# Optimization experiments

Hardware: AMD Instinct MI355X
Metric: run time of the kernel (lower is better)

## Reference

```python
import jax, jax.numpy as jnp
import numpy as np

B, S, H, W, C = 1, 14, 56, 56, 192
WS = 7            # cubic window
SH = 3            # shift
HEADS = 6
HD = C // HEADS
N = WS ** 3       # 343 tokens per window
NW = (S // WS) * (H // WS) * (W // WS)  # 128 windows
SCALE = HD ** -0.5
HID = 4 * C
TBL = (2 * WS - 1) ** 3  # 2197


def _rel_index():
    # faithful to torch: meshgrid with indexing='xy' and the (3*ws-1)/(2*ws-1) strides
    c = np.stack(np.meshgrid(np.arange(WS), np.arange(WS), np.arange(WS), indexing='xy'))
    f = c.reshape(3, -1)                      # (3, N)
    r = (f[:, :, None] - f[:, None, :]).transpose(1, 2, 0)  # (N, N, 3)
    r = r + (WS - 1)
    r[..., 0] *= 3 * WS - 1
    r[..., 1] *= 2 * WS - 1
    return jnp.asarray(r.sum(-1), dtype=jnp.int32)  # (N, N)

REL_IDX = _rel_index()


def _ln(x, g, b):
    m = x.mean(-1, keepdims=True)
    v = ((x - m) ** 2).mean(-1, keepdims=True)
    return (x - m) * jax.lax.rsqrt(v + 1e-5) * g + b


def _partition(x):  # (B,S,H,W,C) -> (B*nW, N, C)
    x = x.reshape(B, S // WS, WS, H // WS, WS, W // WS, WS, C)
    x = x.transpose(0, 1, 3, 5, 2, 4, 6, 7)
    return x.reshape(-1, N, C)


def _reverse(w):  # (B*nW, N, C) -> (B,S,H,W,C)
    x = w.reshape(B, S // WS, H // WS, W // WS, WS, WS, WS, C)
    x = x.transpose(0, 1, 4, 2, 5, 3, 6, 7)
    return x.reshape(B, S, H, W, C)


def setup_inputs() -> dict:
    key = jax.random.key(0)
    ks = jax.random.split(key, 16)
    L = S * H * W
    p = lambda k, shp, s=0.02: (jax.random.normal(k, shp, dtype=jnp.float32) * s)
    return {
        'x': jax.random.normal(ks[0], (B, L, C), dtype=jnp.float32),
        'mask_matrix': jax.random.normal(ks[1], (NW, N, N), dtype=jnp.float32),
        'skip': jax.random.normal(ks[2], (B, L, C), dtype=jnp.float32),
        'x_up': jax.random.normal(ks[3], (B, L, C), dtype=jnp.float32),
        'norm1_g': jnp.ones((C,), jnp.float32),
        'norm1_b': jnp.zeros((C,), jnp.float32),
        'kv_w': p(ks[4], (C, 2 * C)),
        'kv_b': jnp.zeros((2 * C,), jnp.float32),
        'rel_bias_table': p(ks[5], (TBL, HEADS)),
        'proj_w': p(ks[6], (C, C)),
        'proj_b': jnp.zeros((C,), jnp.float32),
        'norm2_g': jnp.ones((C,), jnp.float32),
        'norm2_b': jnp.zeros((C,), jnp.float32),
        'fc1_w': p(ks[7], (C, HID)),
        'fc1_b': jnp.zeros((HID,), jnp.float32),
        'fc2_w': p(ks[8], (HID, C)),
        'fc2_b': jnp.zeros((C,), jnp.float32),
    }


def reference(x, mask_matrix, skip, x_up, norm1_g, norm1_b, kv_w, kv_b,
              rel_bias_table, proj_w, proj_b, norm2_g, norm2_b,
              fc1_w, fc1_b, fc2_w, fc2_b):
    shortcut = x
    sk = _ln(skip, norm1_g, norm1_b).reshape(B, S, H, W, C)
    xu = _ln(x_up, norm1_g, norm1_b).reshape(B, S, H, W, C)
    # cyclic shift (shift_size > 0, dims divisible by window -> no padding)
    sk = jnp.roll(sk, (-SH, -SH, -SH), axis=(1, 2, 3))
    xu = jnp.roll(xu, (-SH, -SH, -SH), axis=(1, 2, 3))
    sk_w = _partition(sk)   # (Bw, N, C)
    xu_w = _partition(xu)
    Bw = sk_w.shape[0]
    kv = (sk_w @ kv_w + kv_b).reshape(Bw, N, 2, HEADS, HD)
    k = kv[:, :, 0].transpose(0, 2, 1, 3)   # (Bw, h, N, d)
    v = kv[:, :, 1].transpose(0, 2, 1, 3)
    q = xu_w.reshape(Bw, N, HEADS, HD).transpose(0, 2, 1, 3) * SCALE
    attn = jnp.einsum('bhnd,bhmd->bhnm', q, k)
    bias = rel_bias_table[REL_IDX].transpose(2, 0, 1)  # (h, N, N)
    attn = attn + bias[None]
    attn = attn.reshape(B, NW, HEADS, N, N) + mask_matrix[None, :, None]
    attn = jax.nn.softmax(attn.reshape(Bw, HEADS, N, N), axis=-1)
    out = jnp.einsum('bhnm,bhmd->bhnd', attn, v)
    out = out.transpose(0, 2, 1, 3).reshape(Bw, N, C)
    out = out @ proj_w + proj_b
    xr = _reverse(out)
    xr = jnp.roll(xr, (SH, SH, SH), axis=(1, 2, 3)).reshape(B, S * H * W, C)
    x = shortcut + xr
    h = _ln(x, norm2_g, norm2_b)
    h = jax.nn.gelu(h @ fc1_w + fc1_b, approximate=False) @ fc2_w + fc2_b
    return x + h
```

## Files before the change

### kernel.cpp

```cpp
#include <hip/hip_runtime.h>
#include <cstddef>

typedef unsigned short u16;
typedef unsigned int   u32;
typedef __bf16 bf16_t;
typedef bf16_t bf16x8 __attribute__((ext_vector_type(8)));
typedef short  s16x4  __attribute__((ext_vector_type(4)));
typedef float  f32x4  __attribute__((ext_vector_type(4)));
typedef u16    u16x4  __attribute__((ext_vector_type(4)));

#define NPAD 352
#define VTS  352
#define LOG2E 1.4426950408889634f
#define RESCALE_THR 11.5f

__device__ __forceinline__ u16 f2b(float f) {
  return __builtin_bit_cast(u16, (__bf16)f);
}
__device__ __forceinline__ float b2f(u16 h) {
  return __uint_as_float(((u32)h) << 16);
}
__device__ __forceinline__ float fexp2(float x) {
#if __has_builtin(__builtin_amdgcn_exp2f)
  return __builtin_amdgcn_exp2f(x);
#else
  float r; asm("v_exp_f32 %0, %1" : "=v"(r) : "v"(x)); return r;
#endif
}
__device__ __forceinline__ f32x4 mfma16(bf16x8 a, bf16x8 b, f32x4 c) {
  return __builtin_amdgcn_mfma_f32_16x16x32_bf16(a, b, c, 0, 0, 0);
}
__device__ __forceinline__ f32x4 mfma16x16(s16x4 a, s16x4 b, f32x4 c) {
#if __has_builtin(__builtin_amdgcn_mfma_f32_16x16x16bf16_1k)
  return __builtin_amdgcn_mfma_f32_16x16x16bf16_1k(a, b, c, 0, 0, 0);
#else
  f32x4 d;
  asm volatile("v_mfma_f32_16x16x16_bf16 %0, %1, %2, %3"
               : "=&v"(d) : "v"(a), "v"(b), "v"(c));
  return d;
#endif
}
__device__ __forceinline__ void gl_lds16(const void* g, void* l) {
  __builtin_amdgcn_global_load_lds((const __attribute__((address_space(1))) void*)g,
                                   (__attribute__((address_space(3))) void*)l, 16, 0, 0);
}

__device__ __forceinline__ int win_to_global(int w, int n) {
  int ws = w >> 6, wh = (w >> 3) & 7, ww = w & 7;
  int ts = (n * 1338) >> 16;
  int rem = n - ts * 49;
  int th = (rem * 9363) >> 16;
  int tw = rem - th * 7;
  int gs = ws * 7 + ts + 3; if (gs >= 14) gs -= 14;
  int gh = wh * 7 + th + 3; if (gh >= 56) gh -= 56;
  int gw = ww * 7 + tw + 3; if (gw >= 56) gw -= 56;
  return (gs * 56 + gh) * 56 + gw;
}

#define MC_END 15488
#define LN_END (MC_END + 10976)
#define WC_END (LN_END + 1824)
#define PRE_GRID (WC_END + 726)

__global__ __launch_bounds__(256) void k_pre(
    const float* __restrict__ mask, u16* __restrict__ mb,
    const float* __restrict__ skip, const float* __restrict__ xup,
    const float* __restrict__ g1, const float* __restrict__ b1,
    u16* __restrict__ skw, u16* __restrict__ qb,
    const float* __restrict__ kv_w, const float* __restrict__ proj_w,
    const float* __restrict__ fc1_w, const float* __restrict__ fc2_w,
    u16* kvT, u16* projT, u16* fc1T, u16* fc2T,
    const float* __restrict__ tbl, u16* __restrict__ bf) {
  int bid = blockIdx.x, tid = threadIdx.x;
  if (bid < MC_END) {
    int t = bid * 256 + tid;
    int w = t / (352 * 88);
    int r = t - w * (352 * 88);
    int n = r / 88;
    int q = r - n * 88;
    u16x4 v = {0, 0, 0, 0};
    if (n < 343) {
      const float* src = mask + ((size_t)w * 343 + n) * 343 + q * 4;
      #pragma unroll
      for (int j = 0; j < 4; ++j) if (q * 4 + j < 343) v[j] = f2b(src[j] * LOG2E);
    }
    *(u16x4*)&mb[((size_t)w * 352 + n) * 352 + q * 4] = v;
  } else if (bid < LN_END) {
    int wid = tid >> 6, lane = tid & 63;
    int m = (bid - MC_END) * 4 + wid;
    u32 w = ((u32)m * 48914u) >> 24;
    int n = m - (int)w * 343;
    int g = win_to_global((int)w, n);
    float xs[3], xu[3];
    float s1 = 0.f, s2 = 0.f, t1 = 0.f, t2 = 0.f;
    #pragma unroll
    for (int i = 0; i < 3; ++i) {
      int c = lane + i * 64;
      xs[i] = skip[(size_t)g * 192 + c];
      xu[i] = xup[(size_t)g * 192 + c];
      s1 += xs[i]; s2 += xs[i] * xs[i];
      t1 += xu[i]; t2 += xu[i] * xu[i];
    }
    #pragma unroll
    for (int off = 1; off < 64; off <<= 1) {
      s1 += __shfl_xor(s1, off); s2 += __shfl_xor(s2, off);
      t1 += __shfl_xor(t1, off); t2 += __shfl_xor(t2, off);
    }
    const float inv = 1.f / 192.f;
    float ms = s1 * inv, vs = s2 * inv - ms * ms;
    float mu = t1 * inv, vu = t2 * inv - mu * mu;
    float rs = rsqrtf(vs + 1e-5f), ru = rsqrtf(vu + 1e-5f);
    #pragma unroll
    for (int i = 0; i < 3; ++i) {
      int c = lane + i * 64;
      float gg = g1[c], bb = b1[c];
      skw[(size_t)m * 192 + c] = f2b((xs[i] - ms) * rs * gg + bb);
      float qv = ((xu[i] - mu) * ru * gg + bb) * 0.25503513f;
      int h = c >> 5, d = c & 31;
      qb[(size_t)(((int)w * 6 + h) * NPAD + n) * 32 + d] = f2b(qv);
    }
  } else if (bid < WC_END) {
    int t = (bid - LN_END) * 256 + tid;
    if (t < 384 * 192) { int nn = t / 192, kk = t - nn * 192; kvT[t] = f2b(kv_w[kk * 384 + nn]); return; }
    t -= 384 * 192;
    if (t < 256 * 192) { int nn = t / 192, kk = t - nn * 192; projT[t] = (nn < 192) ? f2b(proj_w[kk * 192 + nn]) : (u16)0; return; }
    t -= 256 * 192;
    if (t < 768 * 192) { int nn = t / 192, kk = t - nn * 192; fc1T[t] = f2b(fc1_w[kk * 768 + nn]); return; }
    t -= 768 * 192;
    if (t < 256 * 768) { int nn = t / 768, kk = t - nn * 768; fc2T[t] = (nn < 192) ? f2b(fc2_w[kk * 192 + nn]) : (u16)0; return; }
  } else {
    int t = (bid - WC_END) * 256 + tid;
    int h = t / (352 * 88);
    int r = t - h * (352 * 88);
    int n = r / 88;
    int q = r - n * 88;
    u16x4 v = {0, 0, 0, 0};
    if (n < 343 && h < 6) {
      int tsn = (n * 1338) >> 16, remn = n - tsn * 49, thn = (remn * 9363) >> 16, twn = remn - thn * 7;
      #pragma unroll
      for (int j = 0; j < 4; ++j) {
        int m = q * 4 + j;
        if (m < 343) {
          int tsm = (m * 1338) >> 16, remm = m - tsm * 49, thm = (remm * 9363) >> 16, twm = remm - thm * 7;
          int idx = (thn - thm) * 20 + (tsn - tsm) * 13 + (twn - twm) + 204;
          v[j] = f2b(tbl[idx * 6 + h] * LOG2E);
        }
      }
    }
    if (h < 6) *(u16x4*)&bf[((size_t)h * 352 + n) * 352 + q * 4] = v;
  }
}

__global__ __launch_bounds__(256) void k_ln2(const float* __restrict__ xr,
    const float* __restrict__ g2, const float* __restrict__ b2, u16* __restrict__ o) {
  int wid = threadIdx.x >> 6, lane = threadIdx.x & 63;
  int m = blockIdx.x * 4 + wid;
  float v[3]; float s1 = 0.f, s2 = 0.f;
  #pragma unroll
  for (int i = 0; i < 3; ++i) {
    int c = lane + i * 64;
    v[i] = xr[(size_t)m * 192 + c];
    s1 += v[i]; s2 += v[i] * v[i];
  }
  #pragma unroll
  for (int off = 1; off < 64; off <<= 1) { s1 += __shfl_xor(s1, off); s2 += __shfl_xor(s2, off); }
  const float inv = 1.f / 192.f;
  float ms = s1 * inv, vs = s2 * inv - ms * ms;
  float rs = rsqrtf(vs + 1e-5f);
  #pragma unroll
  for (int i = 0; i < 3; ++i) {
    int c = lane + i * 64;
    o[(size_t)m * 192 + c] = f2b((v[i] - ms) * rs * g2[c] + b2[c]);
  }
}

template<int EPI>
__global__ __launch_bounds__(256) void k_gemm(
    const u16* __restrict__ A, const u16* __restrict__ Bm, int K, int nbn,
    const float* __restrict__ bias,
    u16* __restrict__ outa, u16* __restrict__ outb,
    const float* __restrict__ xin, float* __restrict__ xres,
    float* __restrict__ outf) {
  __shared__ __align__(16) u16 As[128 * 64];
  __shared__ __align__(16) u16 Bs[128 * 64];
  int bid = blockIdx.x;
  int xcd = bid & 7, j = bid >> 3;
  int bn = j % nbn, bmL = j / nbn;
  int bm = xcd * 43 + bmL;
  if (bm >= 343) return;
  int tid = threadIdx.x;
  int wid = tid >> 6, lane = tid & 63, lr = lane & 15, lg = lane >> 4;
  int wr = wid >> 1, wc = wid & 1;
  f32x4 acc[4][4] = {};
  const u16* Abase = A + (size_t)bm * 128 * K;
  const u16* Bbase = Bm + (size_t)bn * 128 * K;
  int nk = K >> 6;
  int rsw = lr & 7;
  for (int kt = 0; kt < nk; ++kt) {
    #pragma unroll
    for (int it = 0; it < 4; ++it) {
      int c = it * 256 + tid;
      int row = c >> 3, subp = c & 7;
      int gsub = subp ^ (row & 7);
      gl_lds16(Abase + (size_t)row * K + kt * 64 + gsub * 8, &As[c * 8]);
      gl_lds16(Bbase + (size_t)row * K + kt * 64 + gsub * 8, &Bs[c * 8]);
    }
    __syncthreads();
    #pragma unroll
    for (int kk = 0; kk < 2; ++kk) {
      bf16x8 af[4], bfr[4];
      #pragma unroll
      for (int mi = 0; mi < 4; ++mi)
        af[mi] = *(const bf16x8*)&As[(wr * 64 + mi * 16 + lr) * 64 + ((kk * 4 + lg) ^ rsw) * 8];
      #pragma unroll
      for (int ni = 0; ni < 4; ++ni)
        bfr[ni] = *(const bf16x8*)&Bs[(wc * 64 + ni * 16 + lr) * 64 + ((kk * 4 + lg) ^ rsw) * 8];
      #pragma unroll
      for (int mi = 0; mi < 4; ++mi)
        #pragma unroll
        for (int ni = 0; ni < 4; ++ni)
          acc[mi][ni] = mfma16(af[mi], bfr[ni], acc[mi][ni]);
    }
    __syncthreads();
  }
  #pragma unroll
  for (int mi = 0; mi < 4; ++mi) {
    #pragma unroll
    for (int r = 0; r < 4; ++r) {
      int grow = bm * 128 + wr * 64 + mi * 16 + lg * 4 + r;
      if (EPI == 0) {
        u32 w = ((u32)grow * 48914u) >> 24; int n = grow - (int)w * 343;
        #pragma unroll
        for (int ni = 0; ni < 4; ++ni) {
          int gcol = bn * 128 + wc * 64 + ni * 16 + lr;
          float v = acc[mi][ni][r] + bias[gcol];
          if (gcol < 192) {
            int hh = gcol >> 5, d = gcol & 31;
            int dswz = ((((d >> 3) ^ ((n >> 1) & 3)) << 3) | (d & 7));
            outa[(size_t)(((int)w * 6 + hh) * NPAD + n) * 32 + dswz] = f2b(v);
          } else {
            int c2 = gcol - 192; int hh = c2 >> 5, d = c2 & 31;
            int nswz = ((((n >> 3) ^ ((d >> 1) & 3)) << 3) | (n & 7));
            outb[(size_t)(((int)w * 6 + hh) * 32 + d) * VTS + nswz] = f2b(v);
          }
        }
      } else if (EPI == 1) {
        #pragma unroll
        for (int ni = 0; ni < 4; ++ni) {
          int gcol = bn * 128 + wc * 64 + ni * 16 + lr;
          if (gcol < 192) {
            float v = acc[mi][ni][r] + bias[gcol] + xin[(size_t)grow * 192 + gcol];
            xres[(size_t)grow * 192 + gcol] = v;
          }
        }
      } else if (EPI == 2) {
        #pragma unroll
        for (int ni = 0; ni < 4; ++ni) {
          int gcol = bn * 128 + wc * 64 + ni * 16 + lr;
          float v = acc[mi][ni][r] + bias[gcol];
          v = 0.5f * v * (1.f + erff(v * 0.7071067811865476f));
          outa[(size_t)grow * 768 + gcol] = f2b(v);
        }
      } else {
        #pragma unroll
        for (int ni = 0; ni < 4; ++ni) {
          int gcol = bn * 128 + wc * 64 + ni * 16 + lr;
          if (gcol < 192)
            outf[(size_t)grow * 192 + gcol] = acc[mi][ni][r] + bias[gcol] + xin[(size_t)grow * 192 + gcol];
        }
      }
    }
  }
}

template<int CT0, int LEN, bool TAIL, bool FIRST>
__device__ __forceinline__ void attn_chunk(const u16* __restrict__ Ks, const u16* __restrict__ Vs,
    bf16x8 qa, int lr, int lg, int swz,
    const u16* __restrict__ brow, const u16* __restrict__ mrow,
    f32x4& o0, f32x4& o1, float& mrun, float& sum) {
  u16x4 bb[LEN], mm[LEN];
  #pragma unroll
  for (int j = 0; j < LEN; ++j) {
    bb[j] = *(const u16x4*)&brow[(CT0 + j) * 16];
    mm[j] = *(const u16x4*)&mrow[(CT0 + j) * 16];
  }
  f32x4 s[LEN];
  const f32x4 z = {0.f, 0.f, 0.f, 0.f};
  __builtin_amdgcn_s_setprio(1);
  #pragma unroll
  for (int j = 0; j < LEN; ++j) {
    bf16x8 kf = *(const bf16x8*)&Ks[((CT0 + j) * 16 + lr) * 32 + (lg ^ swz) * 8];
    s[j] = mfma16(kf, qa, z);
  }
  __builtin_amdgcn_s_setprio(0);
  #pragma unroll
  for (int j = 0; j < LEN; ++j)
    #pragma unroll
    for (int r = 0; r < 4; ++r) s[j][r] += b2f(bb[j][r]) + b2f(mm[j][r]);
  if (TAIL) {
    int m0 = 336 + lg * 4;
    #pragma unroll
    for (int r = 0; r < 4; ++r) if (m0 + r >= 343) s[LEN - 1][r] = -1e30f;
  }
  float mloc = -1e30f;
  #pragma unroll
  for (int j = 0; j < LEN; ++j)
    mloc = fmaxf(mloc, fmaxf(fmaxf(s[j][0], s[j][1]), fmaxf(s[j][2], s[j][3])));
  if (FIRST) {
    mloc = fmaxf(mloc, __shfl_xor(mloc, 16));
    mloc = fmaxf(mloc, __shfl_xor(mloc, 32));
    mrun = mloc;
  } else if (!__all(mloc <= mrun + RESCALE_THR)) {
    mloc = fmaxf(mloc, __shfl_xor(mloc, 16));
    mloc = fmaxf(mloc, __shfl_xor(mloc, 32));
    float mnew = fmaxf(mrun, mloc);
    float sc = fexp2(mrun - mnew);
    #pragma unroll
    for (int r = 0; r < 4; ++r) {
      float scr = __shfl(sc, lg * 4 + r);
      o0[r] *= scr; o1[r] *= scr;
    }
    sum *= sc;
    mrun = mnew;
  }
  #pragma unroll
  for (int j = 0; j < LEN; ++j)
    #pragma unroll
    for (int r = 0; r < 4; ++r) { float p = fexp2(s[j][r] - mrun); s[j][r] = p; sum += p; }
  __builtin_amdgcn_s_setprio(1);
  #pragma unroll
  for (int j = 0; j < LEN; ++j) {
    s16x4 pa;
    #pragma unroll
    for (int r = 0; r < 4; ++r) pa[r] = (short)f2b(s[j][r]);
    int c16 = 2 * (CT0 + j) + (lg >> 1);
    int vo = ((c16 ^ swz) * 8) + (lg & 1) * 4;
    s16x4 v0 = *(const s16x4*)&Vs[lr * 352 + vo];
    s16x4 v1 = *(const s16x4*)&Vs[(16 + lr) * 352 + vo];
    o0 = mfma16x16(pa, v0, o0);
    o1 = mfma16x16(pa, v1, o1);
  }
  __builtin_amdgcn_s_setprio(0);
}

__global__ __launch_bounds__(256) void k_attn(const u16* __restrict__ qb, const u16* __restrict__ kb,
    const u16* __restrict__ vtb, const u16* __restrict__ bfull, const u16* __restrict__ maskbf,
    u16* __restrict__ att) {
  __shared__ __align__(16) u16 Ks[352 * 32];
  __shared__ __align__(16) u16 Vs[32 * 352];
  __shared__ __align__(16) u16 Ot[4][16][40];
  int bid = blockIdx.x;
  int xcd = bid & 7, i = bid >> 3;
  int wl = i / 6, h = i - wl * 6;
  int w = xcd * 16 + wl;
  int tid = threadIdx.x, wid = tid >> 6, lane = tid & 63, lr = lane & 15, lg = lane >> 4;
  const u16* Q  = qb  + (size_t)(w * 6 + h) * NPAD * 32;
  const u16* Kg = kb  + (size_t)(w * 6 + h) * NPAD * 32;
  const u16* Vg = vtb + (size_t)(w * 6 + h) * 32 * VTS;
  const u16* Bp = bfull + (size_t)h * 352 * 352;
  const u16* Mp = maskbf + (size_t)w * 352 * 352;
  #pragma unroll
  for (int it = 0; it < 11; ++it) {
    int idx = it * 256 + tid;
    if (idx < 1408) gl_lds16(Kg + idx * 8, &Ks[idx * 8]);
    else            gl_lds16(Vg + (idx - 1408) * 8, &Vs[(idx - 1408) * 8]);
  }
  __syncthreads();
  int swz = (lr >> 1) & 3;
  for (int rt = wid; rt < 22; rt += 4) {
    int n = rt * 16 + lr;
    bf16x8 qa = *(const bf16x8*)&Q[(size_t)n * 32 + lg * 8];
    const u16* brow = Bp + (size_t)n * 352 + lg * 4;
    const u16* mrow = Mp + (size_t)n * 352 + lg * 4;
    f32x4 o0 = {0.f, 0.f, 0.f, 0.f}, o1 = {0.f, 0.f, 0.f, 0.f};
    float mrun = -1e30f, sum = 0.f;
    attn_chunk<0,  6, false, true >(Ks, Vs, qa, lr, lg, swz, brow, mrow, o0, o1, mrun, sum);
    attn_chunk<6,  6, false, false>(Ks, Vs, qa, lr, lg, swz, brow, mrow, o0, o1, mrun, sum);
    attn_chunk<12, 6, false, false>(Ks, Vs, qa, lr, lg, swz, brow, mrow, o0, o1, mrun, sum);
    attn_chunk<18, 4, true,  false>(Ks, Vs, qa, lr, lg, swz, brow, mrow, o0, o1, mrun, sum);
    sum += __shfl_xor(sum, 16);
    sum += __shfl_xor(sum, 32);
    float rs = 1.f / sum;
    #pragma unroll
    for (int r = 0; r < 4; ++r) {
      float rsr = __shfl(rs, lg * 4 + r);
      Ot[wid][lg * 4 + r][lr] = f2b(o0[r] * rsr);
      Ot[wid][lg * 4 + r][16 + lr] = f2b(o1[r] * rsr);
    }
    if (n < 343) {
      int g = win_to_global(w, n);
      bf16x8 ov = *(const bf16x8*)&Ot[wid][lr][lg * 8];
      *(bf16x8*)&att[(size_t)g * 192 + h * 32 + lg * 8] = ov;
    }
  }
}

static const size_t OFF_W    = 0;
static const size_t OFF_XRES = (size_t)1 << 20;
static const size_t OFF_MASK = OFF_XRES;
static const size_t OFF_LN2  = OFF_XRES + ((size_t)34 << 20);
static const size_t OFF_SKW  = OFF_LN2  + ((size_t)17 << 20);
static const size_t OFF_Q    = OFF_SKW  + ((size_t)17 << 20);
static const size_t OFF_K    = OFF_Q    + ((size_t)17 << 20);
static const size_t OFF_VT   = OFF_K    + ((size_t)17 << 20);
static const size_t OFF_ATT  = OFF_VT   + ((size_t)17 << 20);
static const size_t OFF_BIAS = OFF_ATT  + ((size_t)17 << 20);
static const size_t OFF_FC1  = OFF_SKW;

extern "C" void kernel_launch(void* const* d_in, const int* in_sizes, int n_in,
                              void* d_out, int out_size, void* d_ws, size_t ws_size,
                              hipStream_t stream) {
  const float* x      = (const float*)d_in[0];
  const float* mask   = (const float*)d_in[1];
  const float* skip   = (const float*)d_in[2];
  const float* xup    = (const float*)d_in[3];
  const float* n1g    = (const float*)d_in[4];
  const float* n1b    = (const float*)d_in[5];
  const float* kv_w   = (const float*)d_in[6];
  const float* kv_b   = (const float*)d_in[7];
  const float* tbl    = (const float*)d_in[8];
  const float* proj_w = (const float*)d_in[9];
  const float* proj_b = (const float*)d_in[10];
  const float* n2g    = (const float*)d_in[11];
  const float* n2b    = (const float*)d_in[12];
  const float* fc1_w  = (const float*)d_in[13];
  const float* fc1_b  = (const float*)d_in[14];
  const float* fc2_w  = (const float*)d_in[15];
  const float* fc2_b  = (const float*)d_in[16];
  char* ws = (char*)d_ws;
  u16* kvT   = (u16*)(ws + OFF_W);
  u16* projT = kvT + 384 * 192;
  u16* fc1T  = projT + 256 * 192;
  u16* fc2T  = fc1T + 768 * 192;
  float* xres = (float*)(ws + OFF_XRES);
  u16* maskbf = (u16*)(ws + OFF_MASK);
  u16* ln2o  = (u16*)(ws + OFF_LN2);
  u16* skw   = (u16*)(ws + OFF_SKW);
  u16* qb    = (u16*)(ws + OFF_Q);
  u16* kb    = (u16*)(ws + OFF_K);
  u16* vt    = (u16*)(ws + OFF_VT);
  u16* att   = (u16*)(ws + OFF_ATT);
  u16* bfull = (u16*)(ws + OFF_BIAS);
  u16* fc1o  = (u16*)(ws + OFF_FC1);
  float* outp = (float*)d_out;

  k_pre<<<dim3(PRE_GRID), dim3(256), 0, stream>>>(
      mask, maskbf, skip, xup, n1g, n1b, skw, qb,
      kv_w, proj_w, fc1_w, fc2_w, kvT, projT, fc1T, fc2T, tbl, bfull);
  k_gemm<0><<<dim3(8 * 43 * 3), dim3(256), 0, stream>>>(skw, kvT, 192, 3, kv_b, kb, vt, nullptr, nullptr, nullptr);
  k_attn<<<dim3(768), dim3(256), 0, stream>>>(qb, kb, vt, bfull, maskbf, att);
  k_gemm<1><<<dim3(8 * 43 * 2), dim3(256), 0, stream>>>(att, projT, 192, 2, proj_b, nullptr, nullptr, x, xres, nullptr);
  k_ln2<<<dim3(10976), dim3(256), 0, stream>>>(xres, n2g, n2b, ln2o);
  k_gemm<2><<<dim3(8 * 43 * 6), dim3(256), 0, stream>>>(ln2o, fc1T, 192, 6, fc1_b, fc1o, nullptr, nullptr, nullptr, nullptr);
  k_gemm<3><<<dim3(8 * 43 * 2), dim3(256), 0, stream>>>(fc1o, fc2T, 768, 2, fc2_b, nullptr, nullptr, xres, nullptr, outp);
}
```

Measured before the change: 304.7 us.

## Process three query row-tiles per wave to reuse K/V LDS fragments

The attention kernel now has each wave handle three 16-row query tiles at once. Each K and V fragment read from LDS feeds three sets of MFMAs instead of one, and there are more independent MFMA chains to fill the pipeline. The 22 row tiles are split into 7 triples spread across the 4 waves, with the last tile handled singly by wave 3. This raises register pressure (6 accumulators and 3x the bias/mask and score arrays), which may cut occupancy. It also leaves the waves unevenly loaded, since waves 0-2 get two triples while wave 3 gets one triple plus one single tile.

```diff
diff --git a/kernel.cpp b/kernel.cpp
--- a/kernel.cpp
+++ b/kernel.cpp
@@ -343,12 +343,152 @@
   __builtin_amdgcn_s_setprio(0);
 }
 
+template<int CT0, int LEN, bool TAIL, bool FIRST>
+__device__ __forceinline__ void attn_chunk3(const u16* __restrict__ Ks, const u16* __restrict__ Vs,
+    bf16x8 qaA, bf16x8 qaB, bf16x8 qaC, int lr, int lg, int swz,
+    const u16* __restrict__ browA, const u16* __restrict__ mrowA,
+    const u16* __restrict__ browB, const u16* __restrict__ mrowB,
+    const u16* __restrict__ browC, const u16* __restrict__ mrowC,
+    f32x4& o0A, f32x4& o1A, f32x4& o0B, f32x4& o1B, f32x4& o0C, f32x4& o1C,
+    float& mrunA, float& mrunB, float& mrunC, float& sumA, float& sumB, float& sumC) {
+  u16x4 bbA[LEN], mmA[LEN], bbB[LEN], mmB[LEN], bbC[LEN], mmC[LEN];
+  #pragma unroll
+  for (int j = 0; j < LEN; ++j) {
+    bbA[j] = *(const u16x4*)&browA[(CT0 + j) * 16];
+    mmA[j] = *(const u16x4*)&mrowA[(CT0 + j) * 16];
+    bbB[j] = *(const u16x4*)&browB[(CT0 + j) * 16];
+    mmB[j] = *(const u16x4*)&mrowB[(CT0 + j) * 16];
+    bbC[j] = *(const u16x4*)&browC[(CT0 + j) * 16];
+    mmC[j] = *(const u16x4*)&mrowC[(CT0 + j) * 16];
+  }
+  f32x4 sA[LEN], sB[LEN], sC[LEN];
+  const f32x4 z = {0.f, 0.f, 0.f, 0.f};
+  __builtin_amdgcn_s_setprio(1);
+  #pragma unroll
+  for (int j = 0; j < LEN; ++j) {
+    bf16x8 kf = *(const bf16x8*)&Ks[((CT0 + j) * 16 + lr) * 32 + (lg ^ swz) * 8];
+    sA[j] = mfma16(kf, qaA, z);
+    sB[j] = mfma16(kf, qaB, z);
+    sC[j] = mfma16(kf, qaC, z);
+  }
+  __builtin_amdgcn_s_setprio(0);
+  #pragma unroll
+  for (int j = 0; j < LEN; ++j)
+    #pragma unroll
+    for (int r = 0; r < 4; ++r) {
+      sA[j][r] += b2f(bbA[j][r]) + b2f(mmA[j][r]);
+      sB[j][r] += b2f(bbB[j][r]) + b2f(mmB[j][r]);
+      sC[j][r] += b2f(bbC[j][r]) + b2f(mmC[j][r]);
+    }
+  if (TAIL) {
+    int m0 = 336 + lg * 4;
+    #pragma unroll
+    for (int r = 0; r < 4; ++r)
+      if (m0 + r >= 343) { sA[LEN-1][r] = -1e30f; sB[LEN-1][r] = -1e30f; sC[LEN-1][r] = -1e30f; }
+  }
+  float mlA = -1e30f, mlB = -1e30f, mlC = -1e30f;
+  #pragma unroll
+  for (int j = 0; j < LEN; ++j) {
+    mlA = fmaxf(mlA, fmaxf(fmaxf(sA[j][0], sA[j][1]), fmaxf(sA[j][2], sA[j][3])));
+    mlB = fmaxf(mlB, fmaxf(fmaxf(sB[j][0], sB[j][1]), fmaxf(sB[j][2], sB[j][3])));
+    mlC = fmaxf(mlC, fmaxf(fmaxf(sC[j][0], sC[j][1]), fmaxf(sC[j][2], sC[j][3])));
+  }
+  if (FIRST) {
+    mlA = fmaxf(mlA, __shfl_xor(mlA, 16)); mlA = fmaxf(mlA, __shfl_xor(mlA, 32));
+    mlB = fmaxf(mlB, __shfl_xor(mlB, 16)); mlB = fmaxf(mlB, __shfl_xor(mlB, 32));
+    mlC = fmaxf(mlC, __shfl_xor(mlC, 16)); mlC = fmaxf(mlC, __shfl_xor(mlC, 32));
+    mrunA = mlA; mrunB = mlB; mrunC = mlC;
+  } else {
+    if (!__all(mlA <= mrunA + RESCALE_THR)) {
+      mlA = fmaxf(mlA, __shfl_xor(mlA, 16)); mlA = fmaxf(mlA, __shfl_xor(mlA, 32));
+      float mnew = fmaxf(mrunA, mlA);
+      float sc = fexp2(mrunA - mnew);
+      #pragma unroll
+      for (int r = 0; r < 4; ++r) {
+        float scr = __shfl(sc, lg * 4 + r);
+        o0A[r] *= scr; o1A[r] *= scr;
+      }
+      sumA *= sc; mrunA = mnew;
+    }
+    if (!__all(mlB <= mrunB + RESCALE_THR)) {
+      mlB = fmaxf(mlB, __shfl_xor(mlB, 16)); mlB = fmaxf(mlB, __shfl_xor(mlB, 32));
+      float mnew = fmaxf(mrunB, mlB);
+      float sc = fexp2(mrunB - mnew);
+      #pragma unroll
+      for (int r = 0; r < 4; ++r) {
+        float scr = __shfl(sc, lg * 4 + r);
+        o0B[r] *= scr; o1B[r] *= scr;
+      }
+      sumB *= sc; mrunB = mnew;
+    }
+    if (!__all(mlC <= mrunC + RESCALE_THR)) {
+      mlC = fmaxf(mlC, __shfl_xor(mlC, 16)); mlC = fmaxf(mlC, __shfl_xor(mlC, 32));
+      float mnew = fmaxf(mrunC, mlC);
+      float sc = fexp2(mrunC - mnew);
+      #pragma unroll
+      for (int r = 0; r < 4; ++r) {
+        float scr = __shfl(sc, lg * 4 + r);
+        o0C[r] *= scr; o1C[r] *= scr;
+      }
+      sumC *= sc; mrunC = mnew;
+    }
+  }
+  #pragma unroll
+  for (int j = 0; j < LEN; ++j)
+    #pragma unroll
+    for (int r = 0; r < 4; ++r) {
+      float pA = fexp2(sA[j][r] - mrunA); sA[j][r] = pA; sumA += pA;
+      float pB = fexp2(sB[j][r] - mrunB); sB[j][r] = pB; sumB += pB;
+      float pC = fexp2(sC[j][r] - mrunC); sC[j][r] = pC; sumC += pC;
+    }
+  __builtin_amdgcn_s_setprio(1);
+  #pragma unroll
+  for (int j = 0; j < LEN; ++j) {
+    s16x4 paA, paB, paC;
+    #pragma unroll
+    for (int r = 0; r < 4; ++r) {
+      paA[r] = (short)f2b(sA[j][r]);
+      paB[r] = (short)f2b(sB[j][r]);
+      paC[r] = (short)f2b(sC[j][r]);
+    }
+    int c16 = 2 * (CT0 + j) + (lg >> 1);
+    int vo = ((c16 ^ swz) * 8) + (lg & 1) * 4;
+    s16x4 v0 = *(const s16x4*)&Vs[lr * 352 + vo];
+    s16x4 v1 = *(const s16x4*)&Vs[(16 + lr) * 352 + vo];
+    o0A = mfma16x16(paA, v0, o0A);
+    o1A = mfma16x16(paA, v1, o1A);
+    o0B = mfma16x16(paB, v0, o0B);
+    o1B = mfma16x16(paB, v1, o1B);
+    o0C = mfma16x16(paC, v0, o0C);
+    o1C = mfma16x16(paC, v1, o1C);
+  }
+  __builtin_amdgcn_s_setprio(0);
+}
+
+__device__ __forceinline__ void attn_store(u16* OtW, u16* __restrict__ att,
+    int w, int h, int n, int lr, int lg, f32x4 o0, f32x4 o1, float sum, bool guard) {
+  sum += __shfl_xor(sum, 16);
+  sum += __shfl_xor(sum, 32);
+  float rs = 1.f / sum;
+  #pragma unroll
+  for (int r = 0; r < 4; ++r) {
+    float rsr = __shfl(rs, lg * 4 + r);
+    OtW[(lg * 4 + r) * 40 + lr] = f2b(o0[r] * rsr);
+    OtW[(lg * 4 + r) * 40 + 16 + lr] = f2b(o1[r] * rsr);
+  }
+  if (!guard || n < 343) {
+    int g = win_to_global(w, n);
+    bf16x8 ov = *(const bf16x8*)&OtW[lr * 40 + lg * 8];
+    *(bf16x8*)&att[(size_t)g * 192 + h * 32 + lg * 8] = ov;
+  }
+}
+
 __global__ __launch_bounds__(256) void k_attn(const u16* __restrict__ qb, const u16* __restrict__ kb,
     const u16* __restrict__ vtb, const u16* __restrict__ bfull, const u16* __restrict__ maskbf,
     u16* __restrict__ att) {
   __shared__ __align__(16) u16 Ks[352 * 32];
   __shared__ __align__(16) u16 Vs[32 * 352];
-  __shared__ __align__(16) u16 Ot[4][16][40];
+  __shared__ __align__(16) u16 Ot[4][16 * 40];
   int bid = blockIdx.x;
   int xcd = bid & 7, i = bid >> 3;
   int wl = i / 6, h = i - wl * 6;
@@ -367,31 +507,53 @@
   }
   __syncthreads();
   int swz = (lr >> 1) & 3;
-  for (int rt = wid; rt < 22; rt += 4) {
-    int n = rt * 16 + lr;
+  u16* OtW = &Ot[wid][0];
+  for (int t = wid; t <= 6; t += 4) {
+    int nA = (3 * t) * 16 + lr;
+    int nB = nA + 16;
+    int nC = nA + 32;
+    bf16x8 qaA = *(const bf16x8*)&Q[(size_t)nA * 32 + lg * 8];
+    bf16x8 qaB = *(const bf16x8*)&Q[(size_t)nB * 32 + lg * 8];
+    bf16x8 qaC = *(const bf16x8*)&Q[(size_t)nC * 32 + lg * 8];
+    const u16* browA = Bp + (size_t)nA * 352 + lg * 4;
+    const u16* mrowA = Mp + (size_t)nA * 352 + lg * 4;
+    const u16* browB = Bp + (size_t)nB * 352 + lg * 4;
+    const u16* mrowB = Mp + (size_t)nB * 352 + lg * 4;
+    const u16* browC = Bp + (size_t)nC * 352 + lg * 4;
+    const u16* mrowC = Mp + (size_t)nC * 352 + lg * 4;
+    f32x4 o0A = {0.f,0.f,0.f,0.f}, o1A = {0.f,0.f,0.f,0.f};
+    f32x4 o0B = {0.f,0.f,0.f,0.f}, o1B = {0.f,0.f,0.f,0.f};
+    f32x4 o0C = {0.f,0.f,0.f,0.f}, o1C = {0.f,0.f,0.f,0.f};
+    float mrunA = -1e30f, mrunB = -1e30f, mrunC = -1e30f;
+    float sumA = 0.f, sumB = 0.f, sumC = 0.f;
+    attn_chunk3<0,  6, false, true >(Ks, Vs, qaA, qaB, qaC, lr, lg, swz,
+        browA, mrowA, browB, mrowB, browC, mrowC,
+        o0A, o1A, o0B, o1B, o0C, o1C, mrunA, mrunB, mrunC, sumA, sumB, sumC);
+    attn_chunk3<6,  6, false, false>(Ks, Vs, qaA, qaB, qaC, lr, lg, swz,
+        browA, mrowA, browB, mrowB, browC, mrowC,
+        o0A, o1A, o0B, o1B, o0C, o1C, mrunA, mrunB, mrunC, sumA, sumB, sumC);
+    attn_chunk3<12, 6, false, false>(Ks, Vs, qaA, qaB, qaC, lr, lg, swz,
+        browA, mrowA, browB, mrowB, browC, mrowC,
+        o0A, o1A, o0B, o1B, o0C, o1C, mrunA, mrunB, mrunC, sumA, sumB, sumC);
+    attn_chunk3<18, 4, true,  false>(Ks, Vs, qaA, qaB, qaC, lr, lg, swz,
+        browA, mrowA, browB, mrowB, browC, mrowC,
+        o0A, o1A, o0B, o1B, o0C, o1C, mrunA, mrunB, mrunC, sumA, sumB, sumC);
+    attn_store(OtW, att, w, h, nA, lr, lg, o0A, o1A, sumA, false);
+    attn_store(OtW, att, w, h, nB, lr, lg, o0B, o1B, sumB, false);
+    attn_store(OtW, att, w, h, nC, lr, lg, o0C, o1C, sumC, false);
+  }
+  if (wid == 3) {
+    int n = 21 * 16 + lr;
     bf16x8 qa = *(const bf16x8*)&Q[(size_t)n * 32 + lg * 8];
     const u16* brow = Bp + (size_t)n * 352 + lg * 4;
     const u16* mrow = Mp + (size_t)n * 352 + lg * 4;
-    f32x4 o0 = {0.f, 0.f, 0.f, 0.f}, o1 = {0.f, 0.f, 0.f, 0.f};
+    f32x4 o0 = {0.f,0.f,0.f,0.f}, o1 = {0.f,0.f,0.f,0.f};
     float mrun = -1e30f, sum = 0.f;
     attn_chunk<0,  6, false, true >(Ks, Vs, qa, lr, lg, swz, brow, mrow, o0, o1, mrun, sum);
     attn_chunk<6,  6, false, false>(Ks, Vs, qa, lr, lg, swz, brow, mrow, o0, o1, mrun, sum);
     attn_chunk<12, 6, false, false>(Ks, Vs, qa, lr, lg, swz, brow, mrow, o0, o1, mrun, sum);
     attn_chunk<18, 4, true,  false>(Ks, Vs, qa, lr, lg, swz, brow, mrow, o0, o1, mrun, sum);
-    sum += __shfl_xor(sum, 16);
-    sum += __shfl_xor(sum, 32);
-    float rs = 1.f / sum;
-    #pragma unroll
-    for (int r = 0; r < 4; ++r) {
-      float rsr = __shfl(rs, lg * 4 + r);
-      Ot[wid][lg * 4 + r][lr] = f2b(o0[r] * rsr);
-      Ot[wid][lg * 4 + r][16 + lr] = f2b(o1[r] * rsr);
-    }
-    if (n < 343) {
-      int g = win_to_global(w, n);
-      bf16x8 ov = *(const bf16x8*)&Ot[wid][lr][lg * 8];
-      *(bf16x8*)&att[(size_t)g * 192 + h * 32 + lg * 8] = ov;
-    }
+    attn_store(OtW, att, w, h, n, lr, lg, o0, o1, sum, true);
   }
 }
 
```

New measurement: 301.2 us. Within noise of the previous version (-1.1%).
